# Kernel optimization log

Hardware: AMD Instinct MI355X
Metric: run time of the kernel (lower is better)

Reference implementation:

```python
import jax, jax.numpy as jnp
import numpy as np

THRESHOLD = 0.5
NEG_POS = 3
ALPHA = 1.0


def cxcy_to_xy(c):
    return jnp.concatenate([c[..., :2] - c[..., 2:] / 2, c[..., :2] + c[..., 2:] / 2], -1)


def xy_to_cxcy(b):
    return jnp.concatenate([(b[..., :2] + b[..., 2:]) / 2, b[..., 2:] - b[..., :2]], -1)


def compute_iou(a, b):
    # a: (M,4) xyxy, b: (D,4) xyxy -> (M,D)
    lt = jnp.maximum(a[:, None, :2], b[None, :, :2])
    rb = jnp.minimum(a[:, None, 2:], b[None, :, 2:])
    wh = jnp.clip(rb - lt, 0.0)
    inter = wh[..., 0] * wh[..., 1]
    area_a = (a[:, 2] - a[:, 0]) * (a[:, 3] - a[:, 1])
    area_b = (b[:, 2] - b[:, 0]) * (b[:, 3] - b[:, 1])
    return inter / (area_a[:, None] + area_b[None, :] - inter)


def encode_bboxes(g_cxcy, priors_cxcy):
    # standard SSD encoding with variances (0.1, 0.2)
    return jnp.concatenate([
        (g_cxcy[:, :2] - priors_cxcy[:, :2]) / (priors_cxcy[:, 2:] / 10.0),
        jnp.log(g_cxcy[:, 2:] / priors_cxcy[:, 2:]) * 5.0,
    ], -1)


def match_one(boxes, labels, priors_xy, priors_cxcy):
    # boxes: (M,4) xyxy, labels: (M,)
    M = boxes.shape[0]
    overlaps = compute_iou(boxes, priors_xy)                 # (M, D)
    overlaps_per_default = overlaps.max(axis=0)              # (D,)
    objects_per_default = overlaps.argmax(axis=0)            # (D,)
    defaults_per_gt = overlaps.argmax(axis=1)                # (M,)
    # force-match each gt to its best prior
    objects_per_default = objects_per_default.at[defaults_per_gt].set(jnp.arange(M))
    overlaps_per_default = overlaps_per_default.at[defaults_per_gt].set(1.0)
    lab = labels[objects_per_default]                        # (D,)
    lab = jnp.where(overlaps_per_default < THRESHOLD, 0, lab)
    matched = boxes[objects_per_default]                     # (D,4)
    loc_t = encode_bboxes(xy_to_cxcy(matched), priors_cxcy)  # (D,4)
    return loc_t, lab


def setup_inputs() -> dict:
    key = jax.random.key(0)
    ks = jax.random.split(key, 7)
    B, D, M, C = 128, 8732, 32, 21
    p_c = jax.random.uniform(ks[0], (D, 2), minval=0.05, maxval=0.95)
    p_wh = jax.random.uniform(ks[1], (D, 2), minval=0.02, maxval=0.4)
    default_boxes = jnp.concatenate([p_c, p_wh], -1)         # cxcy priors
    g_c = jax.random.uniform(ks[2], (B, M, 2), minval=0.2, maxval=0.8)
    g_wh = jax.random.uniform(ks[3], (B, M, 2), minval=0.05, maxval=0.3)
    gt_boxes = jnp.clip(jnp.concatenate([g_c - g_wh / 2, g_c + g_wh / 2], -1), 0.0, 1.0)
    gt_labels = jax.random.randint(ks[4], (B, M), 1, C)
    loc_pred = jax.random.normal(ks[5], (B, D, 4), dtype=jnp.float32)
    cls_pred = jax.random.normal(ks[6], (B, D, C), dtype=jnp.float32)
    return {"loc_pred": loc_pred, "cls_pred": cls_pred, "gt_boxes": gt_boxes,
            "gt_labels": gt_labels, "default_boxes": default_boxes}


def reference(loc_pred, cls_pred, gt_boxes, gt_labels, default_boxes):
    priors_xy = cxcy_to_xy(default_boxes)
    loc_t, conf_t = jax.vmap(match_one, in_axes=(0, 0, None, None))(
        gt_boxes, gt_labels, priors_xy, default_boxes)      # (B,D,4), (B,D)
    pos = conf_t > 0                                         # (B,D)
    n_pos = pos.sum(axis=1)                                  # (B,)
    n_total = jnp.maximum(n_pos.sum(), 1).astype(loc_pred.dtype)

    # localization: smooth-L1 summed over positives
    d = loc_pred - loc_t
    ad = jnp.abs(d)
    sl1 = jnp.where(ad < 1.0, 0.5 * d * d, ad - 0.5).sum(-1)  # (B,D)
    loc_loss = jnp.where(pos, sl1, 0.0).sum()

    # confidence: CE with hard negative mining (neg:pos = 3)
    logp = jax.nn.log_softmax(cls_pred, axis=-1)
    ce = -jnp.take_along_axis(logp, conf_t[..., None], axis=-1)[..., 0]  # (B,D)
    ce_neg = jnp.where(pos, 0.0, ce)
    order = jnp.argsort(-ce_neg, axis=1)
    rank = jnp.argsort(order, axis=1)                        # hardness rank per row
    n_neg = NEG_POS * n_pos                                  # (B,)
    neg_mask = (rank < n_neg[:, None]) & (~pos)
    conf_loss = jnp.where(pos | neg_mask, ce, 0.0).sum()

    return (conf_loss + ALPHA * loc_loss) / n_total
```

## Files before the change

kernel.cpp:

```cpp
#include <hip/hip_runtime.h>

#define BB 128
#define DD 8732
#define MM 32
#define CC 21

constexpr int K1_PR  = 4;
constexpr int K1_CH  = 256 * K1_PR;
constexpr int K1_NCH = (DD + K1_CH - 1) / K1_CH;
constexpr int K2_CELLS = 256;
constexpr int K2_NBLK  = (DD + K2_CELLS - 1) / K2_CELLS;
constexpr int K2B_T    = 1024;
constexpr int K2B_PER  = (DD + K2B_T - 1) / K2B_T;
constexpr int K2B_W    = K2B_T / 64;

constexpr size_t WS_DPG    = 0;
constexpr size_t WS_ROW    = 32768;
constexpr int    ROW_STRIDE = 16;
constexpr size_t WS_GSUM   = 40960;
constexpr size_t WS_GNPOS  = 41088;
constexpr size_t WS_DONE   = 41216;
constexpr size_t WS_ZERO_BYTES = 41344;
constexpr size_t WS_PACKED = 41472;
constexpr size_t WS_CENEG  = WS_PACKED + (size_t)BB * DD * 4;

__device__ __forceinline__ float wave_sum_f(float v) {
#pragma unroll
  for (int o = 32; o > 0; o >>= 1) v += __shfl_xor(v, o, 64);
  return v;
}
__device__ __forceinline__ int wave_sum_i(int v) {
#pragma unroll
  for (int o = 32; o > 0; o >>= 1) v += __shfl_xor(v, o, 64);
  return v;
}

__global__ __launch_bounds__(256) void k1_match(
    const float* __restrict__ gt_boxes, const int* __restrict__ gt_labels,
    const float* __restrict__ dboxes,
    unsigned int* __restrict__ packed, unsigned long long* __restrict__ dpg) {
  __shared__ float s_gx1[MM], s_gy1[MM], s_gx2[MM], s_gy2[MM], s_ga[MM];
  __shared__ int s_gl[MM];
  __shared__ unsigned long long s_pm[MM * 4];

  const int b = blockIdx.y;
  const int tid = threadIdx.x;
  if (tid < MM) {
    const float* g = gt_boxes + ((size_t)b * MM + tid) * 4;
    const float x1 = g[0], y1 = g[1], x2 = g[2], y2 = g[3];
    s_gx1[tid] = x1; s_gy1[tid] = y1; s_gx2[tid] = x2; s_gy2[tid] = y2;
    s_ga[tid] = __fmul_rn(__fsub_rn(x2, x1), __fsub_rn(y2, y1));
    s_gl[tid] = gt_labels[b * MM + tid];
  }
  __syncthreads();

  float px1[K1_PR], py1[K1_PR], px2[K1_PR], py2[K1_PR], pa[K1_PR];
  int dd[K1_PR];
  const int dbase = blockIdx.x * K1_CH + tid;
#pragma unroll
  for (int i = 0; i < K1_PR; ++i) {
    const int d = dbase + i * 256;
    if (d < DD) {
      const float4 p = *(const float4*)(dboxes + (size_t)d * 4);
      const float hw = __fmul_rn(p.z, 0.5f), hh = __fmul_rn(p.w, 0.5f);
      px1[i] = __fsub_rn(p.x, hw); py1[i] = __fsub_rn(p.y, hh);
      px2[i] = __fadd_rn(p.x, hw); py2[i] = __fadd_rn(p.y, hh);
      pa[i] = __fmul_rn(__fsub_rn(px2[i], px1[i]), __fsub_rn(py2[i], py1[i]));
      dd[i] = d;
    } else {
      px1[i] = 3e9f; py1[i] = 3e9f; px2[i] = 3e9f; py2[i] = 3e9f; pa[i] = 1.0f;
      dd[i] = 0x7FFFFFFF;
    }
  }

  float vb[K1_PR]; int mb[K1_PR];
#pragma unroll
  for (int i = 0; i < K1_PR; ++i) { vb[i] = -1.0f; mb[i] = 0; }

  const int lane = tid & 63, wid = tid >> 6;
  for (int m = 0; m < MM; ++m) {
    const float gx1 = s_gx1[m], gy1 = s_gy1[m], gx2 = s_gx2[m], gy2 = s_gy2[m];
    const float ga = s_ga[m];
    float mv = -1.0f; int md = 0x7FFFFFFF;
#pragma unroll
    for (int i = 0; i < K1_PR; ++i) {
      const float w = fmaxf(0.0f, __fsub_rn(fminf(gx2, px2[i]), fmaxf(gx1, px1[i])));
      const float h = fmaxf(0.0f, __fsub_rn(fminf(gy2, py2[i]), fmaxf(gy1, py1[i])));
      const float inter = __fmul_rn(w, h);
      const float den = __fsub_rn(__fadd_rn(ga, pa[i]), inter);
      const float val = __fdiv_rn(inter, den);
      if (val > vb[i]) { vb[i] = val; mb[i] = m; }
      if (val > mv) { mv = val; md = dd[i]; }
    }
    unsigned long long key =
        (((unsigned long long)__float_as_uint(mv)) << 32) |
        (unsigned long long)(0xFFFFFFFFu - (unsigned)md);
#pragma unroll
    for (int o = 32; o > 0; o >>= 1) {
      const unsigned long long other = __shfl_xor(key, o, 64);
      if (other > key) key = other;
    }
    if (lane == 0) s_pm[m * 4 + wid] = key;
  }
  __syncthreads();
  if (tid < MM) {
    unsigned long long k0 = s_pm[tid * 4 + 0];
    if (s_pm[tid * 4 + 1] > k0) k0 = s_pm[tid * 4 + 1];
    if (s_pm[tid * 4 + 2] > k0) k0 = s_pm[tid * 4 + 2];
    if (s_pm[tid * 4 + 3] > k0) k0 = s_pm[tid * 4 + 3];
    atomicMax(&dpg[b * MM + tid], k0);
  }
#pragma unroll
  for (int i = 0; i < K1_PR; ++i) {
    if (dd[i] < DD) {
      const int lab = (vb[i] < 0.5f) ? 0 : s_gl[mb[i]];
      packed[(size_t)b * DD + dd[i]] = ((unsigned)lab << 8) | (unsigned)mb[i];
    }
  }
}

__global__ __launch_bounds__(256) void k2a_ce(
    const float* __restrict__ loc_pred, const float* __restrict__ cls_pred,
    const float* __restrict__ gt_boxes, const int* __restrict__ gt_labels,
    const float* __restrict__ dboxes, const unsigned int* __restrict__ packed,
    const unsigned long long* __restrict__ dpg, float* __restrict__ ce_neg,
    float* __restrict__ rowacc) {
  __shared__ float s_cls[K2_CELLS * CC];
  __shared__ int s_dstar[MM], s_lab[MM];
  __shared__ float s_gt[MM][4];
  __shared__ float s_rf[4], s_rl[4];
  __shared__ int s_ri[4];

  const int b = blockIdx.y;
  const int d0 = blockIdx.x * K2_CELLS;
  const int tid = threadIdx.x;
  const int ncell = min(K2_CELLS, DD - d0);
  const int nflt = ncell * CC;
  const float* srcf = cls_pred + ((size_t)b * DD + d0) * CC;
  const int nv4 = nflt >> 2;
  for (int i = tid; i < nv4; i += 256)
    ((float4*)s_cls)[i] = ((const float4*)srcf)[i];
  for (int i = (nv4 << 2) + tid; i < nflt; i += 256) s_cls[i] = srcf[i];

  if (tid < MM) {
    s_dstar[tid] = (int)(0xFFFFFFFFu - (unsigned)(dpg[b * MM + tid] & 0xFFFFFFFFull));
    s_lab[tid] = gt_labels[b * MM + tid];
    const float4 g = *(const float4*)(gt_boxes + ((size_t)b * MM + tid) * 4);
    s_gt[tid][0] = g.x; s_gt[tid][1] = g.y; s_gt[tid][2] = g.z; s_gt[tid][3] = g.w;
  }
  __syncthreads();

  float ce_pos = 0.0f, sl1 = 0.0f; int posc = 0;
  if (tid < ncell) {
    const int d = d0 + tid;
    const unsigned p = packed[(size_t)b * DD + d];
    int bm = (int)(p & 255u), lab = (int)(p >> 8);
#pragma unroll
    for (int m = 0; m < MM; ++m)
      if (s_dstar[m] == d) { bm = m; lab = s_lab[m]; }
    const float* x = &s_cls[tid * CC];
    float mx = x[0];
#pragma unroll
    for (int c = 1; c < CC; ++c) mx = fmaxf(mx, x[c]);
    float se = 0.0f;
#pragma unroll
    for (int c = 0; c < CC; ++c) se = __fadd_rn(se, __expf(__fsub_rn(x[c], mx)));
    const float ce = __fsub_rn(__fadd_rn(mx, __logf(se)), x[lab]);
    const bool pos = lab > 0;
    ce_neg[(size_t)b * DD + d] = pos ? -1.0f : ce;
    if (pos) {
      posc = 1; ce_pos = ce;
      const float4 lp = *(const float4*)(loc_pred + ((size_t)b * DD + d) * 4);
      const float4 pr = *(const float4*)(dboxes + (size_t)d * 4);
      const float gx1 = s_gt[bm][0], gy1 = s_gt[bm][1];
      const float gx2 = s_gt[bm][2], gy2 = s_gt[bm][3];
      const float gcx = __fmul_rn(__fadd_rn(gx1, gx2), 0.5f);
      const float gcy = __fmul_rn(__fadd_rn(gy1, gy2), 0.5f);
      const float gw = __fsub_rn(gx2, gx1), gh = __fsub_rn(gy2, gy1);
      const float t0 = __fdiv_rn(__fsub_rn(gcx, pr.x), __fdiv_rn(pr.z, 10.0f));
      const float t1 = __fdiv_rn(__fsub_rn(gcy, pr.y), __fdiv_rn(pr.w, 10.0f));
      const float t2 = __fmul_rn(__logf(__fdiv_rn(gw, pr.z)), 5.0f);
      const float t3 = __fmul_rn(__logf(__fdiv_rn(gh, pr.w)), 5.0f);
      float dv, ad;
      dv = __fsub_rn(lp.x, t0); ad = fabsf(dv);
      sl1 += (ad < 1.0f) ? __fmul_rn(0.5f, __fmul_rn(dv, dv)) : __fsub_rn(ad, 0.5f);
      dv = __fsub_rn(lp.y, t1); ad = fabsf(dv);
      sl1 += (ad < 1.0f) ? __fmul_rn(0.5f, __fmul_rn(dv, dv)) : __fsub_rn(ad, 0.5f);
      dv = __fsub_rn(lp.z, t2); ad = fabsf(dv);
      sl1 += (ad < 1.0f) ? __fmul_rn(0.5f, __fmul_rn(dv, dv)) : __fsub_rn(ad, 0.5f);
      dv = __fsub_rn(lp.w, t3); ad = fabsf(dv);
      sl1 += (ad < 1.0f) ? __fmul_rn(0.5f, __fmul_rn(dv, dv)) : __fsub_rn(ad, 0.5f);
    }
  }
  const float cs = wave_sum_f(ce_pos);
  const float ls = wave_sum_f(sl1);
  const int ps = wave_sum_i(posc);
  const int lane = tid & 63, wid = tid >> 6;
  if (lane == 0) { s_rf[wid] = cs; s_rl[wid] = ls; s_ri[wid] = ps; }
  __syncthreads();
  if (tid == 0) {
    const float c = s_rf[0] + s_rf[1] + s_rf[2] + s_rf[3];
    const float l = s_rl[0] + s_rl[1] + s_rl[2] + s_rl[3];
    const int p = s_ri[0] + s_ri[1] + s_ri[2] + s_ri[3];
    float* row = rowacc + b * ROW_STRIDE;
    atomicAdd(&row[0], c);
    atomicAdd(&row[1], l);
    if (p) atomicAdd((int*)&row[2], p);
  }
}

__global__ __launch_bounds__(K2B_T) void k2b_topk(
    const float* __restrict__ ce_neg, const float* __restrict__ rowacc,
    float* __restrict__ gsum, int* __restrict__ gnpos,
    unsigned int* __restrict__ done, float* __restrict__ out) {
  __shared__ int s_ri[K2B_W];
  __shared__ float s_rf[K2B_W];
  const int b = blockIdx.x;
  const int tid = threadIdx.x;
  const int lane = tid & 63, wid = tid >> 6;
  const float* row = rowacc + b * ROW_STRIDE;
  const int np = ((const int*)row)[2];
  const int k = min(3 * np, DD - np);

  unsigned key[K2B_PER];
#pragma unroll
  for (int i = 0; i < K2B_PER; ++i) {
    const int d = tid + i * K2B_T;
    if (d < DD) {
      const unsigned u = __float_as_uint(ce_neg[(size_t)b * DD + d]);
      key[i] = (u & 0x80000000u) ? ~u : (u | 0x80000000u);
    } else key[i] = 0u;
  }

  float topk_sum = 0.0f;
  if (k > 0) {
    unsigned T = 0u;
    for (int bit = 31; bit >= 0; --bit) {
      const unsigned cand = T | (1u << bit);
      int c = 0;
#pragma unroll
      for (int i = 0; i < K2B_PER; ++i) c += (key[i] >= cand) ? 1 : 0;
      c = wave_sum_i(c);
      if (lane == 0) s_ri[wid] = c;
      __syncthreads();
      int total = 0;
#pragma unroll
      for (int w = 0; w < K2B_W; ++w) total += s_ri[w];
      __syncthreads();
      if (total >= k) T = cand;
    }
    int c = 0; float s = 0.0f;
#pragma unroll
    for (int i = 0; i < K2B_PER; ++i) {
      if (key[i] > T) { c += 1; s += __uint_as_float(key[i] ^ 0x80000000u); }
    }
    c = wave_sum_i(c); s = wave_sum_f(s);
    if (lane == 0) { s_ri[wid] = c; s_rf[wid] = s; }
    __syncthreads();
    if (tid == 0) {
      int cg = 0; float sg = 0.0f;
#pragma unroll
      for (int w = 0; w < K2B_W; ++w) { cg += s_ri[w]; sg += s_rf[w]; }
      const float vT = __uint_as_float(T ^ 0x80000000u);
      topk_sum = sg + (float)(k - cg) * vT;
    }
  }
  if (tid == 0) {
    atomicAdd(gsum, row[0] + row[1] + topk_sum);
    atomicAdd(gnpos, np);
    __threadfence();
    const unsigned old = atomicAdd(done, 1u);
    if (old == BB - 1) {
      const float total = atomicAdd(gsum, 0.0f);
      const int npt = atomicAdd(gnpos, 0);
      const float nt = (float)((npt > 0) ? npt : 1);
      out[0] = __fdiv_rn(total, nt);
    }
  }
}

extern "C" void kernel_launch(void* const* d_in, const int* in_sizes, int n_in,
                              void* d_out, int out_size, void* d_ws, size_t ws_size,
                              hipStream_t stream) {
  const float* loc_pred = (const float*)d_in[0];
  const float* cls_pred = (const float*)d_in[1];
  const float* gt_boxes = (const float*)d_in[2];
  const int* gt_labels = (const int*)d_in[3];
  const float* dboxes = (const float*)d_in[4];

  char* ws = (char*)d_ws;
  unsigned long long* dpg = (unsigned long long*)(ws + WS_DPG);
  float* rowacc = (float*)(ws + WS_ROW);
  float* gsum = (float*)(ws + WS_GSUM);
  int* gnpos = (int*)(ws + WS_GNPOS);
  unsigned int* done = (unsigned int*)(ws + WS_DONE);
  unsigned int* packed = (unsigned int*)(ws + WS_PACKED);
  float* ce_neg = (float*)(ws + WS_CENEG);

  hipMemsetAsync(ws, 0, WS_ZERO_BYTES, stream);

  k1_match<<<dim3(K1_NCH, BB), 256, 0, stream>>>(gt_boxes, gt_labels, dboxes,
                                                 packed, dpg);
  k2a_ce<<<dim3(K2_NBLK, BB), 256, 0, stream>>>(loc_pred, cls_pred, gt_boxes,
                                                gt_labels, dboxes, packed, dpg,
                                                ce_neg, rowacc);
  k2b_topk<<<BB, K2B_T, 0, stream>>>(ce_neg, rowacc, gsum, gnpos, done,
                                     (float*)d_out);
}
```

Measured before the change: 231.6 us.

## Fuse CE and top-k kernels into one per-row kernel keeping keys in registers

Merges the cross-entropy/loc-loss kernel and the top-k selection kernel into one 1024-thread block per batch row. Each block loops over 9 chunks of priors and keeps the negative-CE keys in registers, so the ce_neg round trip through global memory and the rowacc atomics go away. It also adds a shared-memory bitmap to skip the 32-way forced-match scan, double-buffers the radix-select counters to drop one barrier per bit, starts the radix search at bit 30, and reduces the k1 wave argmax with separate float and int shuffles. The cost is that the CE phase now runs on only 128 blocks, which lowers parallelism and memory-level concurrency for the cls_pred read.

```diff
diff --git a/kernel.cpp b/kernel.cpp
--- a/kernel.cpp
+++ b/kernel.cpp
@@ -8,21 +8,18 @@
 constexpr int K1_PR  = 4;
 constexpr int K1_CH  = 256 * K1_PR;
 constexpr int K1_NCH = (DD + K1_CH - 1) / K1_CH;
-constexpr int K2_CELLS = 256;
-constexpr int K2_NBLK  = (DD + K2_CELLS - 1) / K2_CELLS;
-constexpr int K2B_T    = 1024;
-constexpr int K2B_PER  = (DD + K2B_T - 1) / K2B_T;
-constexpr int K2B_W    = K2B_T / 64;
+
+constexpr int K2_T   = 1024;
+constexpr int K2_NC  = (DD + K2_T - 1) / K2_T;
+constexpr int K2_W   = K2_T / 64;
+constexpr int OVW    = (DD + 31) / 32;
 
 constexpr size_t WS_DPG    = 0;
-constexpr size_t WS_ROW    = 32768;
-constexpr int    ROW_STRIDE = 16;
-constexpr size_t WS_GSUM   = 40960;
-constexpr size_t WS_GNPOS  = 41088;
-constexpr size_t WS_DONE   = 41216;
-constexpr size_t WS_ZERO_BYTES = 41344;
-constexpr size_t WS_PACKED = 41472;
-constexpr size_t WS_CENEG  = WS_PACKED + (size_t)BB * DD * 4;
+constexpr size_t WS_GSUM   = 32768;
+constexpr size_t WS_GNPOS  = 32896;
+constexpr size_t WS_DONE   = 33024;
+constexpr size_t WS_ZERO_BYTES = 33152;
+constexpr size_t WS_PACKED = 33280;
 
 __device__ __forceinline__ float wave_sum_f(float v) {
 #pragma unroll
@@ -92,13 +89,16 @@
       if (val > vb[i]) { vb[i] = val; mb[i] = m; }
       if (val > mv) { mv = val; md = dd[i]; }
     }
-    unsigned long long key =
-        (((unsigned long long)__float_as_uint(mv)) << 32) |
-        (unsigned long long)(0xFFFFFFFFu - (unsigned)md);
-#pragma unroll
-    for (int o = 32; o > 0; o >>= 1) {
-      const unsigned long long other = __shfl_xor(key, o, 64);
-      if (other > key) key = other;
+    float wm = mv;
+#pragma unroll
+    for (int o = 32; o > 0; o >>= 1) wm = fmaxf(wm, __shfl_xor(wm, o, 64));
+    unsigned long long key = 0ull;
+    if (wm > 0.0f) {
+      int cd = (mv == wm) ? md : 0x7FFFFFFF;
+#pragma unroll
+      for (int o = 32; o > 0; o >>= 1) cd = min(cd, __shfl_xor(cd, o, 64));
+      key = (((unsigned long long)__float_as_uint(wm)) << 32) |
+            (unsigned long long)(0xFFFFFFFFu - (unsigned)cd);
     }
     if (lane == 0) s_pm[m * 4 + wid] = key;
   }
@@ -108,7 +108,7 @@
     if (s_pm[tid * 4 + 1] > k0) k0 = s_pm[tid * 4 + 1];
     if (s_pm[tid * 4 + 2] > k0) k0 = s_pm[tid * 4 + 2];
     if (s_pm[tid * 4 + 3] > k0) k0 = s_pm[tid * 4 + 3];
-    atomicMax(&dpg[b * MM + tid], k0);
+    if (k0) atomicMax(&dpg[b * MM + tid], k0);
   }
 #pragma unroll
   for (int i = 0; i < K1_PR; ++i) {
@@ -119,154 +119,155 @@
   }
 }
 
-__global__ __launch_bounds__(256) void k2a_ce(
+__global__ __launch_bounds__(K2_T) void k2_fused(
     const float* __restrict__ loc_pred, const float* __restrict__ cls_pred,
     const float* __restrict__ gt_boxes, const int* __restrict__ gt_labels,
     const float* __restrict__ dboxes, const unsigned int* __restrict__ packed,
-    const unsigned long long* __restrict__ dpg, float* __restrict__ ce_neg,
-    float* __restrict__ rowacc) {
-  __shared__ float s_cls[K2_CELLS * CC];
+    const unsigned long long* __restrict__ dpg, float* __restrict__ gsum,
+    int* __restrict__ gnpos, unsigned int* __restrict__ done,
+    float* __restrict__ out) {
+  __shared__ float s_cls[K2_T * CC];
   __shared__ int s_dstar[MM], s_lab[MM];
-  __shared__ float s_gt[MM][4];
-  __shared__ float s_rf[4], s_rl[4];
-  __shared__ int s_ri[4];
-
-  const int b = blockIdx.y;
-  const int d0 = blockIdx.x * K2_CELLS;
-  const int tid = threadIdx.x;
-  const int ncell = min(K2_CELLS, DD - d0);
-  const int nflt = ncell * CC;
-  const float* srcf = cls_pred + ((size_t)b * DD + d0) * CC;
-  const int nv4 = nflt >> 2;
-  for (int i = tid; i < nv4; i += 256)
-    ((float4*)s_cls)[i] = ((const float4*)srcf)[i];
-  for (int i = (nv4 << 2) + tid; i < nflt; i += 256) s_cls[i] = srcf[i];
-
-  if (tid < MM) {
-    s_dstar[tid] = (int)(0xFFFFFFFFu - (unsigned)(dpg[b * MM + tid] & 0xFFFFFFFFull));
-    s_lab[tid] = gt_labels[b * MM + tid];
-    const float4 g = *(const float4*)(gt_boxes + ((size_t)b * MM + tid) * 4);
-    s_gt[tid][0] = g.x; s_gt[tid][1] = g.y; s_gt[tid][2] = g.z; s_gt[tid][3] = g.w;
-  }
-  __syncthreads();
-
-  float ce_pos = 0.0f, sl1 = 0.0f; int posc = 0;
-  if (tid < ncell) {
-    const int d = d0 + tid;
-    const unsigned p = packed[(size_t)b * DD + d];
-    int bm = (int)(p & 255u), lab = (int)(p >> 8);
-#pragma unroll
-    for (int m = 0; m < MM; ++m)
-      if (s_dstar[m] == d) { bm = m; lab = s_lab[m]; }
-    const float* x = &s_cls[tid * CC];
-    float mx = x[0];
-#pragma unroll
-    for (int c = 1; c < CC; ++c) mx = fmaxf(mx, x[c]);
-    float se = 0.0f;
-#pragma unroll
-    for (int c = 0; c < CC; ++c) se = __fadd_rn(se, __expf(__fsub_rn(x[c], mx)));
-    const float ce = __fsub_rn(__fadd_rn(mx, __logf(se)), x[lab]);
-    const bool pos = lab > 0;
-    ce_neg[(size_t)b * DD + d] = pos ? -1.0f : ce;
-    if (pos) {
-      posc = 1; ce_pos = ce;
-      const float4 lp = *(const float4*)(loc_pred + ((size_t)b * DD + d) * 4);
-      const float4 pr = *(const float4*)(dboxes + (size_t)d * 4);
-      const float gx1 = s_gt[bm][0], gy1 = s_gt[bm][1];
-      const float gx2 = s_gt[bm][2], gy2 = s_gt[bm][3];
-      const float gcx = __fmul_rn(__fadd_rn(gx1, gx2), 0.5f);
-      const float gcy = __fmul_rn(__fadd_rn(gy1, gy2), 0.5f);
-      const float gw = __fsub_rn(gx2, gx1), gh = __fsub_rn(gy2, gy1);
-      const float t0 = __fdiv_rn(__fsub_rn(gcx, pr.x), __fdiv_rn(pr.z, 10.0f));
-      const float t1 = __fdiv_rn(__fsub_rn(gcy, pr.y), __fdiv_rn(pr.w, 10.0f));
-      const float t2 = __fmul_rn(__logf(__fdiv_rn(gw, pr.z)), 5.0f);
-      const float t3 = __fmul_rn(__logf(__fdiv_rn(gh, pr.w)), 5.0f);
-      float dv, ad;
-      dv = __fsub_rn(lp.x, t0); ad = fabsf(dv);
-      sl1 += (ad < 1.0f) ? __fmul_rn(0.5f, __fmul_rn(dv, dv)) : __fsub_rn(ad, 0.5f);
-      dv = __fsub_rn(lp.y, t1); ad = fabsf(dv);
-      sl1 += (ad < 1.0f) ? __fmul_rn(0.5f, __fmul_rn(dv, dv)) : __fsub_rn(ad, 0.5f);
-      dv = __fsub_rn(lp.z, t2); ad = fabsf(dv);
-      sl1 += (ad < 1.0f) ? __fmul_rn(0.5f, __fmul_rn(dv, dv)) : __fsub_rn(ad, 0.5f);
-      dv = __fsub_rn(lp.w, t3); ad = fabsf(dv);
-      sl1 += (ad < 1.0f) ? __fmul_rn(0.5f, __fmul_rn(dv, dv)) : __fsub_rn(ad, 0.5f);
-    }
-  }
-  const float cs = wave_sum_f(ce_pos);
-  const float ls = wave_sum_f(sl1);
-  const int ps = wave_sum_i(posc);
-  const int lane = tid & 63, wid = tid >> 6;
-  if (lane == 0) { s_rf[wid] = cs; s_rl[wid] = ls; s_ri[wid] = ps; }
-  __syncthreads();
-  if (tid == 0) {
-    const float c = s_rf[0] + s_rf[1] + s_rf[2] + s_rf[3];
-    const float l = s_rl[0] + s_rl[1] + s_rl[2] + s_rl[3];
-    const int p = s_ri[0] + s_ri[1] + s_ri[2] + s_ri[3];
-    float* row = rowacc + b * ROW_STRIDE;
-    atomicAdd(&row[0], c);
-    atomicAdd(&row[1], l);
-    if (p) atomicAdd((int*)&row[2], p);
-  }
-}
-
-__global__ __launch_bounds__(K2B_T) void k2b_topk(
-    const float* __restrict__ ce_neg, const float* __restrict__ rowacc,
-    float* __restrict__ gsum, int* __restrict__ gnpos,
-    unsigned int* __restrict__ done, float* __restrict__ out) {
-  __shared__ int s_ri[K2B_W];
-  __shared__ float s_rf[K2B_W];
+  __shared__ float4 s_gt[MM];
+  __shared__ unsigned s_ov[OVW];
+  __shared__ int s_bc[2][K2_W];
+  __shared__ float s_f0[K2_W], s_f1[K2_W];
+  __shared__ int s_i0[K2_W];
+  __shared__ float s_rowconf, s_rowloc;
+
   const int b = blockIdx.x;
   const int tid = threadIdx.x;
   const int lane = tid & 63, wid = tid >> 6;
-  const float* row = rowacc + b * ROW_STRIDE;
-  const int np = ((const int*)row)[2];
+
+  for (int i = tid; i < OVW; i += K2_T) s_ov[i] = 0;
+  if (tid < MM) {
+    const int ds = (int)(0xFFFFFFFFu - (unsigned)(dpg[b * MM + tid] & 0xFFFFFFFFull));
+    s_dstar[tid] = ds;
+    s_lab[tid] = gt_labels[b * MM + tid];
+    s_gt[tid] = *(const float4*)(gt_boxes + ((size_t)b * MM + tid) * 4);
+  }
+  __syncthreads();
+  if (tid < MM) {
+    const unsigned ds = (unsigned)s_dstar[tid];
+    if (ds < DD) atomicOr(&s_ov[ds >> 5], 1u << (ds & 31));
+  }
+
+  unsigned key[K2_NC];
+  float cesum = 0.0f, locsum = 0.0f; int posc = 0;
+
+  for (int c = 0; c < K2_NC; ++c) {
+    const int d0 = c * K2_T;
+    const int ncell = min(K2_T, DD - d0);
+    const int nflt = ncell * CC;
+    const float* src = cls_pred + ((size_t)b * DD + d0) * CC;
+    const int nv4 = nflt >> 2;
+    for (int i = tid; i < nv4; i += K2_T)
+      ((float4*)s_cls)[i] = ((const float4*)src)[i];
+    for (int i = (nv4 << 2) + tid; i < nflt; i += K2_T) s_cls[i] = src[i];
+    __syncthreads();
+
+    unsigned kk = 0u;
+    if (tid < ncell) {
+      const int d = d0 + tid;
+      const unsigned p = packed[(size_t)b * DD + d];
+      int bm = (int)(p & 255u), lab = (int)(p >> 8);
+      if ((s_ov[d >> 5] >> (d & 31)) & 1u) {
+#pragma unroll
+        for (int m = 0; m < MM; ++m)
+          if (s_dstar[m] == d) { bm = m; lab = s_lab[m]; }
+      }
+      const float* x = &s_cls[tid * CC];
+      float mx = x[0];
+#pragma unroll
+      for (int c2 = 1; c2 < CC; ++c2) mx = fmaxf(mx, x[c2]);
+      float se = 0.0f;
+#pragma unroll
+      for (int c2 = 0; c2 < CC; ++c2) se = __fadd_rn(se, __expf(__fsub_rn(x[c2], mx)));
+      const float ce = __fsub_rn(__fadd_rn(mx, __logf(se)), x[lab]);
+      if (lab > 0) {
+        posc += 1; cesum += ce;
+        const float4 lp = *(const float4*)(loc_pred + ((size_t)b * DD + d) * 4);
+        const float4 pr = *(const float4*)(dboxes + (size_t)d * 4);
+        const float4 g = s_gt[bm];
+        const float gcx = __fmul_rn(__fadd_rn(g.x, g.z), 0.5f);
+        const float gcy = __fmul_rn(__fadd_rn(g.y, g.w), 0.5f);
+        const float gw = __fsub_rn(g.z, g.x), gh = __fsub_rn(g.w, g.y);
+        const float t0 = __fdiv_rn(__fsub_rn(gcx, pr.x), __fdiv_rn(pr.z, 10.0f));
+        const float t1 = __fdiv_rn(__fsub_rn(gcy, pr.y), __fdiv_rn(pr.w, 10.0f));
+        const float t2 = __fmul_rn(__logf(__fdiv_rn(gw, pr.z)), 5.0f);
+        const float t3 = __fmul_rn(__logf(__fdiv_rn(gh, pr.w)), 5.0f);
+        float dv, ad;
+        dv = __fsub_rn(lp.x, t0); ad = fabsf(dv);
+        locsum += (ad < 1.0f) ? __fmul_rn(0.5f, __fmul_rn(dv, dv)) : __fsub_rn(ad, 0.5f);
+        dv = __fsub_rn(lp.y, t1); ad = fabsf(dv);
+        locsum += (ad < 1.0f) ? __fmul_rn(0.5f, __fmul_rn(dv, dv)) : __fsub_rn(ad, 0.5f);
+        dv = __fsub_rn(lp.z, t2); ad = fabsf(dv);
+        locsum += (ad < 1.0f) ? __fmul_rn(0.5f, __fmul_rn(dv, dv)) : __fsub_rn(ad, 0.5f);
+        dv = __fsub_rn(lp.w, t3); ad = fabsf(dv);
+        locsum += (ad < 1.0f) ? __fmul_rn(0.5f, __fmul_rn(dv, dv)) : __fsub_rn(ad, 0.5f);
+      } else {
+        kk = __float_as_uint(ce) | 0x80000000u;
+      }
+    }
+    key[c] = kk;
+    __syncthreads();
+  }
+
+  {
+    const int ps = wave_sum_i(posc);
+    const float cs = wave_sum_f(cesum);
+    const float ls = wave_sum_f(locsum);
+    if (lane == 0) { s_i0[wid] = ps; s_f0[wid] = cs; s_f1[wid] = ls; }
+  }
+  __syncthreads();
+  int np = 0;
+#pragma unroll
+  for (int w = 0; w < K2_W; ++w) np += s_i0[w];
+  if (tid == 0) {
+    float cg = 0.0f, lg = 0.0f;
+#pragma unroll
+    for (int w = 0; w < K2_W; ++w) { cg += s_f0[w]; lg += s_f1[w]; }
+    s_rowconf = cg; s_rowloc = lg;
+  }
   const int k = min(3 * np, DD - np);
-
-  unsigned key[K2B_PER];
-#pragma unroll
-  for (int i = 0; i < K2B_PER; ++i) {
-    const int d = tid + i * K2B_T;
-    if (d < DD) {
-      const unsigned u = __float_as_uint(ce_neg[(size_t)b * DD + d]);
-      key[i] = (u & 0x80000000u) ? ~u : (u | 0x80000000u);
-    } else key[i] = 0u;
-  }
+  __syncthreads();
 
   float topk_sum = 0.0f;
   if (k > 0) {
-    unsigned T = 0u;
-    for (int bit = 31; bit >= 0; --bit) {
+    unsigned T = 0x80000000u;
+    int par = 0;
+    for (int bit = 30; bit >= 0; --bit) {
       const unsigned cand = T | (1u << bit);
       int c = 0;
 #pragma unroll
-      for (int i = 0; i < K2B_PER; ++i) c += (key[i] >= cand) ? 1 : 0;
+      for (int i = 0; i < K2_NC; ++i) c += (key[i] >= cand) ? 1 : 0;
       c = wave_sum_i(c);
-      if (lane == 0) s_ri[wid] = c;
+      if (lane == 0) s_bc[par][wid] = c;
       __syncthreads();
       int total = 0;
 #pragma unroll
-      for (int w = 0; w < K2B_W; ++w) total += s_ri[w];
-      __syncthreads();
+      for (int w = 0; w < K2_W; ++w) total += s_bc[par][w];
       if (total >= k) T = cand;
+      par ^= 1;
     }
     int c = 0; float s = 0.0f;
 #pragma unroll
-    for (int i = 0; i < K2B_PER; ++i) {
+    for (int i = 0; i < K2_NC; ++i) {
       if (key[i] > T) { c += 1; s += __uint_as_float(key[i] ^ 0x80000000u); }
     }
     c = wave_sum_i(c); s = wave_sum_f(s);
-    if (lane == 0) { s_ri[wid] = c; s_rf[wid] = s; }
+    if (lane == 0) { s_i0[wid] = c; s_f0[wid] = s; }
     __syncthreads();
     if (tid == 0) {
       int cg = 0; float sg = 0.0f;
 #pragma unroll
-      for (int w = 0; w < K2B_W; ++w) { cg += s_ri[w]; sg += s_rf[w]; }
+      for (int w = 0; w < K2_W; ++w) { cg += s_i0[w]; sg += s_f0[w]; }
       const float vT = __uint_as_float(T ^ 0x80000000u);
       topk_sum = sg + (float)(k - cg) * vT;
     }
   }
   if (tid == 0) {
-    atomicAdd(gsum, row[0] + row[1] + topk_sum);
+    atomicAdd(gsum, s_rowconf + s_rowloc + topk_sum);
     atomicAdd(gnpos, np);
     __threadfence();
     const unsigned old = atomicAdd(done, 1u);
@@ -290,20 +291,16 @@
 
   char* ws = (char*)d_ws;
   unsigned long long* dpg = (unsigned long long*)(ws + WS_DPG);
-  float* rowacc = (float*)(ws + WS_ROW);
   float* gsum = (float*)(ws + WS_GSUM);
   int* gnpos = (int*)(ws + WS_GNPOS);
   unsigned int* done = (unsigned int*)(ws + WS_DONE);
   unsigned int* packed = (unsigned int*)(ws + WS_PACKED);
-  float* ce_neg = (float*)(ws + WS_CENEG);
 
   hipMemsetAsync(ws, 0, WS_ZERO_BYTES, stream);
 
   k1_match<<<dim3(K1_NCH, BB), 256, 0, stream>>>(gt_boxes, gt_labels, dboxes,
                                                  packed, dpg);
-  k2a_ce<<<dim3(K2_NBLK, BB), 256, 0, stream>>>(loc_pred, cls_pred, gt_boxes,
-                                                gt_labels, dboxes, packed, dpg,
-                                                ce_neg, rowacc);
-  k2b_topk<<<BB, K2B_T, 0, stream>>>(ce_neg, rowacc, gsum, gnpos, done,
-                                     (float*)d_out);
-}
+  k2_fused<<<BB, K2_T, 0, stream>>>(loc_pred, cls_pred, gt_boxes, gt_labels,
+                                    dboxes, packed, dpg, gsum, gnpos, done,
+                                    (float*)d_out);
+}
```

Measured after the change: 253.7 us. 9.5% more time.
